# Kernel tuning notes

Hardware: AMD Instinct MI355X
Metric: run time of the kernel (lower is better)

## Reference

```python
import jax, jax.numpy as jnp
import numpy as np

B, T, E, H = 8, 1024, 256, 8
TEMP = E ** 0.5


def setup_inputs() -> dict:
    key = jax.random.key(0)
    ks = jax.random.split(key, 7)
    x = jax.random.normal(ks[0], (B, T, E), dtype=jnp.float32)
    # boolean mask: True = masked position (masked_fill with -inf)
    mask = jax.random.randint(ks[1], (B, T, T), 0, 2) > 0
    s_in = 1.0 / np.sqrt(E)
    s_fc = 1.0 / np.sqrt(H * E)
    Wq = jax.random.normal(ks[2], (E, H * E), dtype=jnp.float32) * s_in
    Wk = jax.random.normal(ks[3], (E, H * E), dtype=jnp.float32) * s_in
    Wv = jax.random.normal(ks[4], (E, H * E), dtype=jnp.float32) * s_in
    Wfc = jax.random.normal(ks[5], (H * E, E), dtype=jnp.float32) * s_fc
    bfc = jax.random.normal(ks[6], (E,), dtype=jnp.float32) * s_fc
    return {"x": x, "Wq": Wq, "Wk": Wk, "Wv": Wv, "Wfc": Wfc, "bfc": bfc, "mask": mask}


def reference(x, Wq, Wk, Wv, Wfc, bfc, mask):
    b, t, e = x.shape
    h = H
    # QKV projections -> [b, t, h, e] (per-head dim == emb_dim here)
    q = (x @ Wq).reshape(b, t, h, e)
    k = (x @ Wk).reshape(b, t, h, e)
    v = (x @ Wv).reshape(b, t, h, e)
    # scores: [b, h, q, k]
    attn = jnp.einsum('bqhe,bkhe->bhqk', q / TEMP, k)
    attn = jnp.where(mask[:, None, :, :], -jnp.inf, attn)
    attn = jax.nn.softmax(attn, axis=-1)
    # rows fully masked give NaN -> replaced by 0 (masked_fill(attn != attn, 0))
    attn = jnp.where(jnp.isnan(attn), 0.0, attn)
    out = jnp.einsum('bhqk,bkhe->bqhe', attn, v).reshape(b, t, h * e)
    return out @ Wfc + bfc
```

## Files before the change

kernel.cpp:

```cpp
#include <hip/hip_runtime.h>


typedef __attribute__((ext_vector_type(8))) short bf16x8;
typedef __attribute__((ext_vector_type(4))) float f32x4;
typedef __attribute__((ext_vector_type(4))) unsigned short u16x4;
typedef __attribute__((ext_vector_type(2))) unsigned int u32x2;
typedef __attribute__((ext_vector_type(4))) int i32x4;

#define B_DIM 8
#define T_DIM 1024
#define E_DIM 256
#define H_DIM 8

__device__ __forceinline__ unsigned short f2bf(float f) {
  unsigned u = __builtin_bit_cast(unsigned, f);
  u += 0x7FFFu + ((u >> 16) & 1u);
  return (unsigned short)(u >> 16);
}

__device__ __forceinline__ void gload_lds16(const void* g, void* l) {
  __builtin_amdgcn_global_load_lds(
      (const __attribute__((address_space(1))) void*)g,
      (__attribute__((address_space(3))) void*)l, 16, 0, 0);
}

__device__ __forceinline__ f32x4 mfma16(bf16x8 a, bf16x8 b, f32x4 c) {
  return __builtin_amdgcn_mfma_f32_16x16x32_bf16(a, b, c, 0, 0, 0);
}

__global__ __launch_bounds__(256) void xcast_kernel(const float* __restrict__ in,
                                                    unsigned short* __restrict__ out,
                                                    int n4) {
  int i = blockIdx.x * 256 + threadIdx.x;
  if (i >= n4) return;
  f32x4 v = ((const f32x4*)in)[i];
  u16x4 o = { f2bf(v[0]), f2bf(v[1]), f2bf(v[2]), f2bf(v[3]) };
  ((u16x4*)out)[i] = o;
}

__global__ __launch_bounds__(256) void mpack_kernel(const int* __restrict__ m,
                                                    unsigned char* __restrict__ out,
                                                    int n8) {
  int i = blockIdx.x * 256 + threadIdx.x;
  if (i >= n8) return;
  i32x4 a = ((const i32x4*)m)[i * 2];
  i32x4 b = ((const i32x4*)m)[i * 2 + 1];
  unsigned v = 0;
  v |= (a[0] != 0) ? 1u : 0u;
  v |= (a[1] != 0) ? 2u : 0u;
  v |= (a[2] != 0) ? 4u : 0u;
  v |= (a[3] != 0) ? 8u : 0u;
  v |= (b[0] != 0) ? 16u : 0u;
  v |= (b[1] != 0) ? 32u : 0u;
  v |= (b[2] != 0) ? 64u : 0u;
  v |= (b[3] != 0) ? 128u : 0u;
  out[i] = (unsigned char)v;
}

__global__ __launch_bounds__(256) void wtrans_kernel(const float* __restrict__ in,
                                                     unsigned short* __restrict__ out,
                                                     int K, int N) {
  __shared__ unsigned short tile[64][65];
  int n0 = blockIdx.x * 64, k0 = blockIdx.y * 64;
  int tid = threadIdx.x;
#pragma unroll
  for (int p = 0; p < 16; ++p) {
    int i = p * 256 + tid;
    int r = i >> 6, c = i & 63;
    tile[c][r] = f2bf(in[(size_t)(k0 + r) * N + n0 + c]);
  }
  __syncthreads();
#pragma unroll
  for (int p = 0; p < 16; ++p) {
    int i = p * 256 + tid;
    int r = i >> 6, c = i & 63;
    out[(size_t)(n0 + r) * K + k0 + c] = tile[r][c];
  }
}

template <int MODE>
__global__ __launch_bounds__(256) void gemm_kernel(
    const unsigned short* __restrict__ A, const unsigned short* __restrict__ BT,
    const float* __restrict__ bias, void* __restrict__ Cout,
    int M, int N, int K, float scale) {
  __shared__ unsigned short As[128 * 64];
  __shared__ unsigned short Bs[128 * 64];
  const int tid = threadIdx.x;
  const int w = tid >> 6, l = tid & 63, lg = l >> 4, lr = l & 15;
  const int tn = blockIdx.x * 128, tm = blockIdx.y * 128;
  const int wm = (w >> 1) * 64, wn = (w & 1) * 64;

  f32x4 acc[4][4];
#pragma unroll
  for (int i = 0; i < 4; ++i)
#pragma unroll
    for (int j = 0; j < 4; ++j) acc[i][j] = (f32x4){0.f, 0.f, 0.f, 0.f};

  for (int kt = 0; kt < K; kt += 64) {
#pragma unroll
    for (int j = 0; j < 4; ++j) {
      int d = j * 4096 + w * 1024 + l * 16;
      int row = d >> 7, cb = d & 127;
      gload_lds16((const char*)(A + (size_t)(tm + row) * K + kt) + (cb ^ ((row & 7) << 4)),
                  (char*)As + j * 4096 + w * 1024);
    }
#pragma unroll
    for (int j = 0; j < 4; ++j) {
      int d = j * 4096 + w * 1024 + l * 16;
      int row = d >> 7, cb = d & 127;
      gload_lds16((const char*)(BT + (size_t)(tn + row) * K + kt) + (cb ^ ((row & 7) << 4)),
                  (char*)Bs + j * 4096 + w * 1024);
    }
    __syncthreads();
#pragma unroll
    for (int c = 0; c < 2; ++c) {
      bf16x8 af[4], bfr[4];
#pragma unroll
      for (int mf = 0; mf < 4; ++mf) {
        int row = wm + mf * 16 + lr;
        af[mf] = *(const bf16x8*)((const char*)As + row * 128 +
                                  ((c * 64 + lg * 16) ^ ((row & 7) << 4)));
      }
#pragma unroll
      for (int nf = 0; nf < 4; ++nf) {
        int row = wn + nf * 16 + lr;
        bfr[nf] = *(const bf16x8*)((const char*)Bs + row * 128 +
                                   ((c * 64 + lg * 16) ^ ((row & 7) << 4)));
      }
#pragma unroll
      for (int mf = 0; mf < 4; ++mf)
#pragma unroll
        for (int nf = 0; nf < 4; ++nf)
          acc[mf][nf] = mfma16(af[mf], bfr[nf], acc[mf][nf]);
    }
    __syncthreads();
  }

#pragma unroll
  for (int mf = 0; mf < 4; ++mf) {
#pragma unroll
    for (int nf = 0; nf < 4; ++nf) {
      int col = tn + wn + nf * 16 + lr;
      int row0 = tm + wm + mf * 16 + lg * 4;
      if constexpr (MODE == 0) {
        float bv = bias[col];
        float* C = (float*)Cout;
#pragma unroll
        for (int r = 0; r < 4; ++r)
          C[(size_t)(row0 + r) * N + col] = acc[mf][nf][r] * scale + bv;
      } else if constexpr (MODE == 1) {
        unsigned short* C = (unsigned short*)Cout;
#pragma unroll
        for (int r = 0; r < 4; ++r) {
          int rowm = row0 + r;
          int bi = rowm >> 10, t = rowm & 1023, hh = col >> 8, e = col & 255;
          C[(((size_t)bi * H_DIM + hh) * T_DIM + t) * E_DIM + e] =
              f2bf(acc[mf][nf][r] * scale);
        }
      } else {
        unsigned short* C = (unsigned short*)Cout;
        int bi = row0 >> 10, t0 = row0 & 1023, hh = col >> 8, e = col & 255;
        u16x4 pk = { f2bf(acc[mf][nf][0] * scale), f2bf(acc[mf][nf][1] * scale),
                     f2bf(acc[mf][nf][2] * scale), f2bf(acc[mf][nf][3] * scale) };
        *(u16x4*)&C[(((size_t)bi * H_DIM + hh) * E_DIM + e) * T_DIM + t0] = pk;
      }
    }
  }
}

__global__ __launch_bounds__(512) void attn_kernel(
    const unsigned short* __restrict__ qb, const unsigned short* __restrict__ kb,
    const unsigned short* __restrict__ vtb,
    const unsigned long long* __restrict__ mpk,
    unsigned short* __restrict__ aout) {
  __shared__ unsigned short Kt[2][64 * 256];
  __shared__ unsigned short Vt[2][256 * 64];
  __shared__ unsigned short Pt[8][16 * 64];

  const int tid = threadIdx.x;
  const int w = tid >> 6, l = tid & 63, lg = l >> 4, lr = l & 15;
  const int bid = blockIdx.x;
  const int x = bid & 7, j = bid >> 3;
  const int bh = x * 8 + (j >> 3), qt = j & 7;
  const int b = bh >> 3, h = bh & 7;

  const unsigned short* qg = qb + (size_t)bh * T_DIM * E_DIM + (size_t)(qt * 128) * E_DIM;
  const unsigned short* kg = kb + (size_t)bh * T_DIM * E_DIM;
  const char* vgc = (const char*)(vtb + (size_t)bh * E_DIM * T_DIM);
  const unsigned long long* mrow =
      mpk + ((size_t)b * T_DIM + qt * 128 + w * 16 + lr) * 16;

  auto stageKV = [&](int bufi, int kt) {
    const char* ksrc = (const char*)(kg + (size_t)(kt * 64) * E_DIM);
    char* kdst = (char*)Kt[bufi];
    char* vdst = (char*)Vt[bufi];
#pragma unroll
    for (int j2 = 0; j2 < 4; ++j2) {
      int d = j2 * 8192 + w * 1024 + l * 16;
      int row = d >> 9, cb = d & 511;
      gload_lds16(ksrc + row * 512 + (cb ^ ((row & 7) << 4)), kdst + d);
    }
#pragma unroll
    for (int j2 = 0; j2 < 4; ++j2) {
      int d = j2 * 8192 + w * 1024 + l * 16;
      int row = d >> 7, cb = d & 127;
      gload_lds16(vgc + (size_t)row * 2048 + kt * 128 + (cb ^ ((row & 7) << 4)),
                  vdst + d);
    }
  };

  stageKV(0, 0);
  bf16x8 qf[8];
  {
    const unsigned short* qrow = qg + (size_t)(w * 16 + lr) * E_DIM + lg * 8;
#pragma unroll
    for (int c = 0; c < 8; ++c) qf[c] = *(const bf16x8*)(qrow + c * 32);
  }

  f32x4 O[16];
#pragma unroll
  for (int i = 0; i < 16; ++i) O[i] = (f32x4){0.f, 0.f, 0.f, 0.f};
  float m_run = -INFINITY, l_run = 0.f;

  __syncthreads();

  for (int kt = 0; kt < 16; ++kt) {
    const int cur = kt & 1;
    unsigned long long m64 = mrow[kt];
    if (kt < 15) stageKV(cur ^ 1, kt + 1);

    f32x4 S[4];
#pragma unroll
    for (int i = 0; i < 4; ++i) S[i] = (f32x4){0.f, 0.f, 0.f, 0.f};
    __builtin_amdgcn_s_setprio(1);
#pragma unroll
    for (int kvf = 0; kvf < 4; ++kvf) {
      int row = kvf * 16 + lr;
      const char* abase = (const char*)Kt[cur] + row * 512;
      int swz = (row & 7) << 4;
#pragma unroll
      for (int c = 0; c < 8; ++c) {
        bf16x8 a = *(const bf16x8*)(abase + ((c * 64 + lg * 16) ^ swz));
        S[kvf] = mfma16(a, qf[c], S[kvf]);
      }
    }
    __builtin_amdgcn_s_setprio(0);

    float p[4][4];
    float tmax = -INFINITY;
#pragma unroll
    for (int kvf = 0; kvf < 4; ++kvf) {
      unsigned nib = (unsigned)(m64 >> (kvf * 16 + lg * 4)) & 0xFu;
#pragma unroll
      for (int r = 0; r < 4; ++r) {
        float sv = S[kvf][r];
        if (nib & (1u << r)) sv = -INFINITY;
        p[kvf][r] = sv;
        tmax = fmaxf(tmax, sv);
      }
    }
    tmax = fmaxf(tmax, __shfl_xor(tmax, 16, 64));
    tmax = fmaxf(tmax, __shfl_xor(tmax, 32, 64));
    float m_new = fmaxf(m_run, tmax);
    float msafe = fmaxf(m_new, -1e30f);
    float alpha = __expf(m_run - msafe);
    float rsum = 0.f;
#pragma unroll
    for (int kvf = 0; kvf < 4; ++kvf)
#pragma unroll
      for (int r = 0; r < 4; ++r) {
        float e = __expf(p[kvf][r] - msafe);
        p[kvf][r] = e;
        rsum += e;
      }
    rsum += __shfl_xor(rsum, 16, 64);
    rsum += __shfl_xor(rsum, 32, 64);
    l_run = l_run * alpha + rsum;
    m_run = m_new;

    {
      char* pb = (char*)(Pt[w]) + lr * 128;
      int swz = (lr & 7) << 4;
#pragma unroll
      for (int kvf = 0; kvf < 4; ++kvf) {
        u32x2 pk;
        pk[0] = (unsigned)f2bf(p[kvf][0]) | ((unsigned)f2bf(p[kvf][1]) << 16);
        pk[1] = (unsigned)f2bf(p[kvf][2]) | ((unsigned)f2bf(p[kvf][3]) << 16);
        *(u32x2*)(pb + ((kvf * 32 + lg * 8) ^ swz)) = pk;
      }
    }

    {
      float av0 = __shfl(alpha, lg * 4 + 0, 64);
      float av1 = __shfl(alpha, lg * 4 + 1, 64);
      float av2 = __shfl(alpha, lg * 4 + 2, 64);
      float av3 = __shfl(alpha, lg * 4 + 3, 64);
#pragma unroll
      for (int nf = 0; nf < 16; ++nf) {
        O[nf][0] *= av0; O[nf][1] *= av1; O[nf][2] *= av2; O[nf][3] *= av3;
      }
    }

    __builtin_amdgcn_s_setprio(1);
#pragma unroll
    for (int c2 = 0; c2 < 2; ++c2) {
      const char* pbase = (const char*)(Pt[w]) + lr * 128;
      bf16x8 pa = *(const bf16x8*)(pbase + ((c2 * 64 + lg * 16) ^ ((lr & 7) << 4)));
#pragma unroll
      for (int nf = 0; nf < 16; ++nf) {
        int vrow = nf * 16 + lr;
        bf16x8 vb = *(const bf16x8*)((const char*)Vt[cur] + vrow * 128 +
                                     ((c2 * 64 + lg * 16) ^ ((vrow & 7) << 4)));
        O[nf] = mfma16(pa, vb, O[nf]);
      }
    }
    __builtin_amdgcn_s_setprio(0);

    __syncthreads();
  }

  float lv[4];
#pragma unroll
  for (int r = 0; r < 4; ++r) {
    float lval = __shfl(l_run, lg * 4 + r, 64);
    lv[r] = lval > 0.f ? 1.f / lval : 0.f;
  }
  const int qrow0 = qt * 128 + w * 16 + lg * 4;
  unsigned short* obase = aout + (size_t)(b * T_DIM) * 2048 + h * 256;
#pragma unroll
  for (int nf = 0; nf < 16; ++nf) {
#pragma unroll
    for (int r = 0; r < 4; ++r) {
      obase[(size_t)(qrow0 + r) * 2048 + nf * 16 + lr] = f2bf(O[nf][r] * lv[r]);
    }
  }
}

extern "C" void kernel_launch(void* const* d_in, const int* in_sizes, int n_in,
                              void* d_out, int out_size, void* d_ws, size_t ws_size,
                              hipStream_t stream) {
  (void)in_sizes; (void)n_in; (void)out_size; (void)ws_size;
  const float* x    = (const float*)d_in[0];
  const float* Wq   = (const float*)d_in[1];
  const float* Wk   = (const float*)d_in[2];
  const float* Wv   = (const float*)d_in[3];
  const float* Wfc  = (const float*)d_in[4];
  const float* bfc  = (const float*)d_in[5];
  const int* mask   = (const int*)d_in[6];
  float* out = (float*)d_out;

  char* ws = (char*)d_ws;
  unsigned short* xbf  = (unsigned short*)(ws + 0);
  unsigned short* qbuf = (unsigned short*)(ws + 4194304);
  unsigned short* kbuf = (unsigned short*)(ws + 37748736);
  unsigned short* vbuf = (unsigned short*)(ws + 71303168);
  unsigned short* abuf = (unsigned short*)(ws + 104857600);
  unsigned short* wqT  = (unsigned short*)(ws + 138412032);
  unsigned short* wkT  = (unsigned short*)(ws + 139460608);
  unsigned short* wvT  = (unsigned short*)(ws + 140509184);
  unsigned short* wfcT = (unsigned short*)(ws + 141557760);
  unsigned char*  mpk  = (unsigned char*)(ws + 142606336);

  xcast_kernel<<<2048, 256, 0, stream>>>(x, xbf, 524288);
  mpack_kernel<<<4096, 256, 0, stream>>>(mask, mpk, 1048576);
  wtrans_kernel<<<dim3(32, 4), 256, 0, stream>>>(Wq, wqT, 256, 2048);
  wtrans_kernel<<<dim3(32, 4), 256, 0, stream>>>(Wk, wkT, 256, 2048);
  wtrans_kernel<<<dim3(32, 4), 256, 0, stream>>>(Wv, wvT, 256, 2048);
  wtrans_kernel<<<dim3(4, 32), 256, 0, stream>>>(Wfc, wfcT, 2048, 256);

  gemm_kernel<1><<<dim3(16, 64), 256, 0, stream>>>(xbf, wqT, nullptr, qbuf,
                                                   8192, 2048, 256, 1.0f / 16.0f);
  gemm_kernel<1><<<dim3(16, 64), 256, 0, stream>>>(xbf, wkT, nullptr, kbuf,
                                                   8192, 2048, 256, 1.0f);
  gemm_kernel<2><<<dim3(16, 64), 256, 0, stream>>>(xbf, wvT, nullptr, vbuf,
                                                   8192, 2048, 256, 1.0f);

  attn_kernel<<<512, 512, 0, stream>>>(qbuf, kbuf, vbuf,
                                       (const unsigned long long*)mpk, abuf);

  gemm_kernel<0><<<dim3(2, 64), 256, 0, stream>>>(abuf, wfcT, bfc, out,
                                                  8192, 256, 2048, 1.0f);
}
```

Before: 314.7 us.

## Merge prep and QKV launches, add lazy softmax rescale, single-buffer attention, retile FC GEMM

Fuses the x cast and mask pack into one prep kernel and the four weight transposes into one launch. The Q/K/V projections become a single GEMM over a concatenated weight, with the 1/TEMP scale split as 0.25 into both Wq and Wk. Attention drops the K/V double buffer for a single buffer loaded after each tile, raising occupancy at the cost of load/compute overlap. It also skips the online-softmax rescale unless the row max grows by more than 8. The FC GEMM moves to 64x64 tiles to launch more blocks, and the reduced launch count cuts per-launch overhead.

```diff
diff --git a/kernel.cpp b/kernel.cpp
--- a/kernel.cpp
+++ b/kernel.cpp
@@ -28,46 +28,55 @@
   return __builtin_amdgcn_mfma_f32_16x16x32_bf16(a, b, c, 0, 0, 0);
 }
 
-__global__ __launch_bounds__(256) void xcast_kernel(const float* __restrict__ in,
-                                                    unsigned short* __restrict__ out,
-                                                    int n4) {
-  int i = blockIdx.x * 256 + threadIdx.x;
-  if (i >= n4) return;
-  f32x4 v = ((const f32x4*)in)[i];
-  u16x4 o = { f2bf(v[0]), f2bf(v[1]), f2bf(v[2]), f2bf(v[3]) };
-  ((u16x4*)out)[i] = o;
-}
-
-__global__ __launch_bounds__(256) void mpack_kernel(const int* __restrict__ m,
-                                                    unsigned char* __restrict__ out,
-                                                    int n8) {
-  int i = blockIdx.x * 256 + threadIdx.x;
-  if (i >= n8) return;
-  i32x4 a = ((const i32x4*)m)[i * 2];
-  i32x4 b = ((const i32x4*)m)[i * 2 + 1];
-  unsigned v = 0;
-  v |= (a[0] != 0) ? 1u : 0u;
-  v |= (a[1] != 0) ? 2u : 0u;
-  v |= (a[2] != 0) ? 4u : 0u;
-  v |= (a[3] != 0) ? 8u : 0u;
-  v |= (b[0] != 0) ? 16u : 0u;
-  v |= (b[1] != 0) ? 32u : 0u;
-  v |= (b[2] != 0) ? 64u : 0u;
-  v |= (b[3] != 0) ? 128u : 0u;
-  out[i] = (unsigned char)v;
-}
-
-__global__ __launch_bounds__(256) void wtrans_kernel(const float* __restrict__ in,
-                                                     unsigned short* __restrict__ out,
-                                                     int K, int N) {
+__global__ __launch_bounds__(256) void prep_kernel(
+    const float* __restrict__ x, unsigned short* __restrict__ xbf,
+    const int* __restrict__ mask, unsigned* __restrict__ mpk) {
+  int bid = blockIdx.x;
+  if (bid < 2048) {
+    int i = bid * 256 + threadIdx.x;
+    f32x4 v = ((const f32x4*)x)[i];
+    u16x4 o = { f2bf(v[0]), f2bf(v[1]), f2bf(v[2]), f2bf(v[3]) };
+    ((u16x4*)xbf)[i] = o;
+  } else {
+    int i = (bid - 2048) * 256 + threadIdx.x;
+    const i32x4* src = (const i32x4*)(mask + (size_t)i * 32);
+    unsigned v = 0;
+#pragma unroll
+    for (int j = 0; j < 8; ++j) {
+      i32x4 a = src[j];
+      v |= (a[0] != 0 ? 1u : 0u) << (j * 4 + 0);
+      v |= (a[1] != 0 ? 1u : 0u) << (j * 4 + 1);
+      v |= (a[2] != 0 ? 1u : 0u) << (j * 4 + 2);
+      v |= (a[3] != 0 ? 1u : 0u) << (j * 4 + 3);
+    }
+    mpk[i] = v;
+  }
+}
+
+__global__ __launch_bounds__(256) void wtrans_all(
+    const float* __restrict__ Wq, const float* __restrict__ Wk,
+    const float* __restrict__ Wv, const float* __restrict__ Wfc,
+    unsigned short* __restrict__ wall, unsigned short* __restrict__ wfcT) {
   __shared__ unsigned short tile[64][65];
-  int n0 = blockIdx.x * 64, k0 = blockIdx.y * 64;
-  int tid = threadIdx.x;
+  const int which = blockIdx.y, bx = blockIdx.x, tid = threadIdx.x;
+  const float* in;
+  unsigned short* out;
+  int K, N, n0, k0;
+  float scale;
+  if (which < 3) {
+    in = which == 0 ? Wq : (which == 1 ? Wk : Wv);
+    out = wall + (size_t)which * 2048 * 256;
+    K = 256; N = 2048; scale = which == 2 ? 1.0f : 0.25f;
+    n0 = (bx & 31) * 64; k0 = (bx >> 5) * 64;
+  } else {
+    in = Wfc; out = wfcT; K = 2048; N = 256; scale = 1.0f;
+    n0 = (bx & 3) * 64; k0 = (bx >> 2) * 64;
+  }
 #pragma unroll
   for (int p = 0; p < 16; ++p) {
     int i = p * 256 + tid;
     int r = i >> 6, c = i & 63;
-    tile[c][r] = f2bf(in[(size_t)(k0 + r) * N + n0 + c]);
+    tile[c][r] = f2bf(in[(size_t)(k0 + r) * N + n0 + c] * scale);
   }
   __syncthreads();
 #pragma unroll
@@ -78,11 +87,9 @@
   }
 }
 
-template <int MODE>
-__global__ __launch_bounds__(256) void gemm_kernel(
+__global__ __launch_bounds__(256) void gemm_qkv(
     const unsigned short* __restrict__ A, const unsigned short* __restrict__ BT,
-    const float* __restrict__ bias, void* __restrict__ Cout,
-    int M, int N, int K, float scale) {
+    unsigned short* __restrict__ qk, unsigned short* __restrict__ vout) {
   __shared__ unsigned short As[128 * 64];
   __shared__ unsigned short Bs[128 * 64];
   const int tid = threadIdx.x;
@@ -96,20 +103,20 @@
 #pragma unroll
     for (int j = 0; j < 4; ++j) acc[i][j] = (f32x4){0.f, 0.f, 0.f, 0.f};
 
-  for (int kt = 0; kt < K; kt += 64) {
+  for (int kt = 0; kt < 256; kt += 64) {
 #pragma unroll
     for (int j = 0; j < 4; ++j) {
       int d = j * 4096 + w * 1024 + l * 16;
       int row = d >> 7, cb = d & 127;
-      gload_lds16((const char*)(A + (size_t)(tm + row) * K + kt) + (cb ^ ((row & 7) << 4)),
-                  (char*)As + j * 4096 + w * 1024);
+      gload_lds16((const char*)(A + (size_t)(tm + row) * 256 + kt) + (cb ^ ((row & 7) << 4)),
+                  (char*)As + d);
     }
 #pragma unroll
     for (int j = 0; j < 4; ++j) {
       int d = j * 4096 + w * 1024 + l * 16;
       int row = d >> 7, cb = d & 127;
-      gload_lds16((const char*)(BT + (size_t)(tn + row) * K + kt) + (cb ^ ((row & 7) << 4)),
-                  (char*)Bs + j * 4096 + w * 1024);
+      gload_lds16((const char*)(BT + (size_t)(tn + row) * 256 + kt) + (cb ^ ((row & 7) << 4)),
+                  (char*)Bs + d);
     }
     __syncthreads();
 #pragma unroll
@@ -136,45 +143,43 @@
     __syncthreads();
   }
 
-#pragma unroll
-  for (int mf = 0; mf < 4; ++mf) {
-#pragma unroll
-    for (int nf = 0; nf < 4; ++nf) {
-      int col = tn + wn + nf * 16 + lr;
-      int row0 = tm + wm + mf * 16 + lg * 4;
-      if constexpr (MODE == 0) {
-        float bv = bias[col];
-        float* C = (float*)Cout;
-#pragma unroll
-        for (int r = 0; r < 4; ++r)
-          C[(size_t)(row0 + r) * N + col] = acc[mf][nf][r] * scale + bv;
-      } else if constexpr (MODE == 1) {
-        unsigned short* C = (unsigned short*)Cout;
+  if (tn < 4096) {
+#pragma unroll
+    for (int mf = 0; mf < 4; ++mf)
+#pragma unroll
+      for (int nf = 0; nf < 4; ++nf) {
+        int col = tn + wn + nf * 16 + lr;
+        int row0 = tm + wm + mf * 16 + lg * 4;
+        int h16 = col >> 8, e = col & 255;
 #pragma unroll
         for (int r = 0; r < 4; ++r) {
           int rowm = row0 + r;
-          int bi = rowm >> 10, t = rowm & 1023, hh = col >> 8, e = col & 255;
-          C[(((size_t)bi * H_DIM + hh) * T_DIM + t) * E_DIM + e] =
-              f2bf(acc[mf][nf][r] * scale);
+          int bi = rowm >> 10, t = rowm & 1023;
+          qk[(((size_t)bi * 16 + h16) * T_DIM + t) * E_DIM + e] = f2bf(acc[mf][nf][r]);
         }
-      } else {
-        unsigned short* C = (unsigned short*)Cout;
-        int bi = row0 >> 10, t0 = row0 & 1023, hh = col >> 8, e = col & 255;
-        u16x4 pk = { f2bf(acc[mf][nf][0] * scale), f2bf(acc[mf][nf][1] * scale),
-                     f2bf(acc[mf][nf][2] * scale), f2bf(acc[mf][nf][3] * scale) };
-        *(u16x4*)&C[(((size_t)bi * H_DIM + hh) * E_DIM + e) * T_DIM + t0] = pk;
-      }
-    }
-  }
-}
-
-__global__ __launch_bounds__(512) void attn_kernel(
-    const unsigned short* __restrict__ qb, const unsigned short* __restrict__ kb,
-    const unsigned short* __restrict__ vtb,
+      }
+  } else {
+#pragma unroll
+    for (int mf = 0; mf < 4; ++mf)
+#pragma unroll
+      for (int nf = 0; nf < 4; ++nf) {
+        int col = tn + wn + nf * 16 + lr;
+        int row0 = tm + wm + mf * 16 + lg * 4;
+        int bi = row0 >> 10, t0 = row0 & 1023;
+        int hh = (col >> 8) - 16, e = col & 255;
+        u16x4 pk = { f2bf(acc[mf][nf][0]), f2bf(acc[mf][nf][1]),
+                     f2bf(acc[mf][nf][2]), f2bf(acc[mf][nf][3]) };
+        *(u16x4*)&vout[(((size_t)bi * H_DIM + hh) * E_DIM + e) * T_DIM + t0] = pk;
+      }
+  }
+}
+
+__global__ __launch_bounds__(512, 4) void attn_kernel(
+    const unsigned short* __restrict__ qkb, const unsigned short* __restrict__ vtb,
     const unsigned long long* __restrict__ mpk,
     unsigned short* __restrict__ aout) {
-  __shared__ unsigned short Kt[2][64 * 256];
-  __shared__ unsigned short Vt[2][256 * 64];
+  __shared__ unsigned short Kt[64 * 256];
+  __shared__ unsigned short Vt[256 * 64];
   __shared__ unsigned short Pt[8][16 * 64];
 
   const int tid = threadIdx.x;
@@ -184,32 +189,31 @@
   const int bh = x * 8 + (j >> 3), qt = j & 7;
   const int b = bh >> 3, h = bh & 7;
 
-  const unsigned short* qg = qb + (size_t)bh * T_DIM * E_DIM + (size_t)(qt * 128) * E_DIM;
-  const unsigned short* kg = kb + (size_t)bh * T_DIM * E_DIM;
+  const unsigned short* qg =
+      qkb + (((size_t)b * 16 + h) * T_DIM + qt * 128) * E_DIM;
+  const unsigned short* kg = qkb + (((size_t)b * 16 + 8 + h) * T_DIM) * E_DIM;
   const char* vgc = (const char*)(vtb + (size_t)bh * E_DIM * T_DIM);
   const unsigned long long* mrow =
       mpk + ((size_t)b * T_DIM + qt * 128 + w * 16 + lr) * 16;
 
-  auto stageKV = [&](int bufi, int kt) {
+  auto stageKV = [&](int kt) {
     const char* ksrc = (const char*)(kg + (size_t)(kt * 64) * E_DIM);
-    char* kdst = (char*)Kt[bufi];
-    char* vdst = (char*)Vt[bufi];
 #pragma unroll
     for (int j2 = 0; j2 < 4; ++j2) {
       int d = j2 * 8192 + w * 1024 + l * 16;
       int row = d >> 9, cb = d & 511;
-      gload_lds16(ksrc + row * 512 + (cb ^ ((row & 7) << 4)), kdst + d);
+      gload_lds16(ksrc + row * 512 + (cb ^ ((row & 7) << 4)), (char*)Kt + d);
     }
 #pragma unroll
     for (int j2 = 0; j2 < 4; ++j2) {
       int d = j2 * 8192 + w * 1024 + l * 16;
       int row = d >> 7, cb = d & 127;
       gload_lds16(vgc + (size_t)row * 2048 + kt * 128 + (cb ^ ((row & 7) << 4)),
-                  vdst + d);
+                  (char*)Vt + d);
     }
   };
 
-  stageKV(0, 0);
+  stageKV(0);
   bf16x8 qf[8];
   {
     const unsigned short* qrow = qg + (size_t)(w * 16 + lr) * E_DIM + lg * 8;
@@ -222,12 +226,9 @@
   for (int i = 0; i < 16; ++i) O[i] = (f32x4){0.f, 0.f, 0.f, 0.f};
   float m_run = -INFINITY, l_run = 0.f;
 
-  __syncthreads();
-
   for (int kt = 0; kt < 16; ++kt) {
-    const int cur = kt & 1;
     unsigned long long m64 = mrow[kt];
-    if (kt < 15) stageKV(cur ^ 1, kt + 1);
+    __syncthreads();
 
     f32x4 S[4];
 #pragma unroll
@@ -236,7 +237,7 @@
 #pragma unroll
     for (int kvf = 0; kvf < 4; ++kvf) {
       int row = kvf * 16 + lr;
-      const char* abase = (const char*)Kt[cur] + row * 512;
+      const char* abase = (const char*)Kt + row * 512;
       int swz = (row & 7) << 4;
 #pragma unroll
       for (int c = 0; c < 8; ++c) {
@@ -261,9 +262,12 @@
     }
     tmax = fmaxf(tmax, __shfl_xor(tmax, 16, 64));
     tmax = fmaxf(tmax, __shfl_xor(tmax, 32, 64));
-    float m_new = fmaxf(m_run, tmax);
-    float msafe = fmaxf(m_new, -1e30f);
-    float alpha = __expf(m_run - msafe);
+
+    float m_old = m_run;
+    int full = !__all(tmax - m_run <= 8.0f);
+    if (full) m_run = fmaxf(m_run, tmax);
+    float msafe = fmaxf(m_run, -1e30f);
+
     float rsum = 0.f;
 #pragma unroll
     for (int kvf = 0; kvf < 4; ++kvf)
@@ -275,8 +279,21 @@
       }
     rsum += __shfl_xor(rsum, 16, 64);
     rsum += __shfl_xor(rsum, 32, 64);
-    l_run = l_run * alpha + rsum;
-    m_run = m_new;
+
+    if (full) {
+      float alpha = __expf(m_old - msafe);
+      float av0 = __shfl(alpha, lg * 4 + 0, 64);
+      float av1 = __shfl(alpha, lg * 4 + 1, 64);
+      float av2 = __shfl(alpha, lg * 4 + 2, 64);
+      float av3 = __shfl(alpha, lg * 4 + 3, 64);
+#pragma unroll
+      for (int nf = 0; nf < 16; ++nf) {
+        O[nf][0] *= av0; O[nf][1] *= av1; O[nf][2] *= av2; O[nf][3] *= av3;
+      }
+      l_run = l_run * alpha + rsum;
+    } else {
+      l_run += rsum;
+    }
 
     {
       char* pb = (char*)(Pt[w]) + lr * 128;
@@ -290,17 +307,6 @@
       }
     }
 
-    {
-      float av0 = __shfl(alpha, lg * 4 + 0, 64);
-      float av1 = __shfl(alpha, lg * 4 + 1, 64);
-      float av2 = __shfl(alpha, lg * 4 + 2, 64);
-      float av3 = __shfl(alpha, lg * 4 + 3, 64);
-#pragma unroll
-      for (int nf = 0; nf < 16; ++nf) {
-        O[nf][0] *= av0; O[nf][1] *= av1; O[nf][2] *= av2; O[nf][3] *= av3;
-      }
-    }
-
     __builtin_amdgcn_s_setprio(1);
 #pragma unroll
     for (int c2 = 0; c2 < 2; ++c2) {
@@ -309,7 +315,7 @@
 #pragma unroll
       for (int nf = 0; nf < 16; ++nf) {
         int vrow = nf * 16 + lr;
-        bf16x8 vb = *(const bf16x8*)((const char*)Vt[cur] + vrow * 128 +
+        bf16x8 vb = *(const bf16x8*)((const char*)Vt + vrow * 128 +
                                      ((c2 * 64 + lg * 16) ^ ((vrow & 7) << 4)));
         O[nf] = mfma16(pa, vb, O[nf]);
       }
@@ -317,6 +323,7 @@
     __builtin_amdgcn_s_setprio(0);
 
     __syncthreads();
+    if (kt < 15) stageKV(kt + 1);
   }
 
   float lv[4];
@@ -334,6 +341,75 @@
       obase[(size_t)(qrow0 + r) * 2048 + nf * 16 + lr] = f2bf(O[nf][r] * lv[r]);
     }
   }
+}
+
+__global__ __launch_bounds__(256) void gemm_fc(
+    const unsigned short* __restrict__ A, const unsigned short* __restrict__ BT,
+    const float* __restrict__ bias, float* __restrict__ C) {
+  __shared__ unsigned short As[64 * 64];
+  __shared__ unsigned short Bs[64 * 64];
+  const int tid = threadIdx.x;
+  const int w = tid >> 6, l = tid & 63, lg = l >> 4, lr = l & 15;
+  const int tn = blockIdx.x * 64, tm = blockIdx.y * 64;
+  const int wm = (w >> 1) * 32, wn = (w & 1) * 32;
+
+  f32x4 acc[2][2];
+#pragma unroll
+  for (int i = 0; i < 2; ++i)
+#pragma unroll
+    for (int j = 0; j < 2; ++j) acc[i][j] = (f32x4){0.f, 0.f, 0.f, 0.f};
+
+  for (int kt = 0; kt < 2048; kt += 64) {
+#pragma unroll
+    for (int j = 0; j < 2; ++j) {
+      int d = j * 4096 + (tid & 255) * 16;
+      int row = d >> 7, cb = d & 127;
+      gload_lds16((const char*)(A + (size_t)(tm + row) * 2048 + kt) + (cb ^ ((row & 7) << 4)),
+                  (char*)As + d);
+    }
+#pragma unroll
+    for (int j = 0; j < 2; ++j) {
+      int d = j * 4096 + (tid & 255) * 16;
+      int row = d >> 7, cb = d & 127;
+      gload_lds16((const char*)(BT + (size_t)(tn + row) * 2048 + kt) + (cb ^ ((row & 7) << 4)),
+                  (char*)Bs + d);
+    }
+    __syncthreads();
+#pragma unroll
+    for (int c = 0; c < 2; ++c) {
+      bf16x8 af[2], bfr[2];
+#pragma unroll
+      for (int mf = 0; mf < 2; ++mf) {
+        int row = wm + mf * 16 + lr;
+        af[mf] = *(const bf16x8*)((const char*)As + row * 128 +
+                                  ((c * 64 + lg * 16) ^ ((row & 7) << 4)));
+      }
+#pragma unroll
+      for (int nf = 0; nf < 2; ++nf) {
+        int row = wn + nf * 16 + lr;
+        bfr[nf] = *(const bf16x8*)((const char*)Bs + row * 128 +
+                                   ((c * 64 + lg * 16) ^ ((row & 7) << 4)));
+      }
+#pragma unroll
+      for (int mf = 0; mf < 2; ++mf)
+#pragma unroll
+        for (int nf = 0; nf < 2; ++nf)
+          acc[mf][nf] = mfma16(af[mf], bfr[nf], acc[mf][nf]);
+    }
+    __syncthreads();
+  }
+
+#pragma unroll
+  for (int mf = 0; mf < 2; ++mf)
+#pragma unroll
+    for (int nf = 0; nf < 2; ++nf) {
+      int col = tn + wn + nf * 16 + lr;
+      int row0 = tm + wm + mf * 16 + lg * 4;
+      float bv = bias[col];
+#pragma unroll
+      for (int r = 0; r < 4; ++r)
+        C[(size_t)(row0 + r) * 256 + col] = acc[mf][nf][r] + bv;
+    }
 }
 
 extern "C" void kernel_launch(void* const* d_in, const int* in_sizes, int n_in,
@@ -351,33 +427,17 @@
 
   char* ws = (char*)d_ws;
   unsigned short* xbf  = (unsigned short*)(ws + 0);
-  unsigned short* qbuf = (unsigned short*)(ws + 4194304);
-  unsigned short* kbuf = (unsigned short*)(ws + 37748736);
+  unsigned short* qkb  = (unsigned short*)(ws + 4194304);
   unsigned short* vbuf = (unsigned short*)(ws + 71303168);
   unsigned short* abuf = (unsigned short*)(ws + 104857600);
-  unsigned short* wqT  = (unsigned short*)(ws + 138412032);
-  unsigned short* wkT  = (unsigned short*)(ws + 139460608);
-  unsigned short* wvT  = (unsigned short*)(ws + 140509184);
+  unsigned short* wall = (unsigned short*)(ws + 138412032);
   unsigned short* wfcT = (unsigned short*)(ws + 141557760);
-  unsigned char*  mpk  = (unsigned char*)(ws + 142606336);
-
-  xcast_kernel<<<2048, 256, 0, stream>>>(x, xbf, 524288);
-  mpack_kernel<<<4096, 256, 0, stream>>>(mask, mpk, 1048576);
-  wtrans_kernel<<<dim3(32, 4), 256, 0, stream>>>(Wq, wqT, 256, 2048);
-  wtrans_kernel<<<dim3(32, 4), 256, 0, stream>>>(Wk, wkT, 256, 2048);
-  wtrans_kernel<<<dim3(32, 4), 256, 0, stream>>>(Wv, wvT, 256, 2048);
-  wtrans_kernel<<<dim3(4, 32), 256, 0, stream>>>(Wfc, wfcT, 2048, 256);
-
-  gemm_kernel<1><<<dim3(16, 64), 256, 0, stream>>>(xbf, wqT, nullptr, qbuf,
-                                                   8192, 2048, 256, 1.0f / 16.0f);
-  gemm_kernel<1><<<dim3(16, 64), 256, 0, stream>>>(xbf, wkT, nullptr, kbuf,
-                                                   8192, 2048, 256, 1.0f);
-  gemm_kernel<2><<<dim3(16, 64), 256, 0, stream>>>(xbf, wvT, nullptr, vbuf,
-                                                   8192, 2048, 256, 1.0f);
-
-  attn_kernel<<<512, 512, 0, stream>>>(qbuf, kbuf, vbuf,
+  unsigned*       mpk  = (unsigned*)(ws + 142606336);
+
+  prep_kernel<<<3072, 256, 0, stream>>>(x, xbf, mask, mpk);
+  wtrans_all<<<dim3(128, 4), 256, 0, stream>>>(Wq, Wk, Wv, Wfc, wall, wfcT);
+  gemm_qkv<<<dim3(48, 64), 256, 0, stream>>>(xbf, wall, qkb, vbuf);
+  attn_kernel<<<512, 512, 0, stream>>>(qkb, vbuf,
                                        (const unsigned long long*)mpk, abuf);
-
-  gemm_kernel<0><<<dim3(2, 64), 256, 0, stream>>>(abuf, wfcT, bfc, out,
-                                                  8192, 256, 2048, 1.0f);
-}
+  gemm_fc<<<dim3(4, 128), 256, 0, stream>>>(abuf, wfcT, bfc, out);
+}
```

Measured after the change: 410.7 us. 1.31x slower.
